# Optimization experiments

Measured on AMD Instinct MI355X. Metric: run time of the kernel, lower is better.

The kernel has to match this reference:

```python
import jax, jax.numpy as jnp
import numpy as np

N = 100000   # nodes
D = 64       # padded neighbor-list width (avg degree)
F = 256      # in_channels
H = 256      # hidden_channels
E = 131072   # number of target edges
OUT = 1      # out_channels


def _linear_params(key, fin, fout):
    k1, k2 = jax.random.split(key)
    s = 1.0 / np.sqrt(fin)
    w = jax.random.uniform(k1, (fin, fout), jnp.float32, -s, s)
    b = jax.random.uniform(k2, (fout,), jnp.float32, -s, s)
    return w, b


def setup_inputs() -> dict:
    key = jax.random.key(0)
    ks = jax.random.split(key, 12)
    x = jax.random.normal(ks[0], (N, F), jnp.float32)
    # sorted padded neighbor lists: row i -> D neighbor ids (sorted, as in the
    # bit-packed sorted-element representation the torch code intersects)
    neighbors = jnp.sort(jax.random.randint(ks[1], (N, D), 0, N), axis=1).astype(jnp.int32)
    tar_ei = jax.random.randint(ks[2], (2, E), 0, N).astype(jnp.int32)
    cn_w1, cn_b1 = _linear_params(ks[3], 1, H)
    cn_w2, cn_b2 = _linear_params(ks[4], H, H)
    cn_w3, cn_b3 = _linear_params(ks[5], H, H)
    ij_w1, ij_b1 = _linear_params(ks[6], F, H)
    ij_w2, ij_b2 = _linear_params(ks[7], H, H)
    lin_w1, lin_b1 = _linear_params(ks[8], H, H)
    lin_w2, lin_b2 = _linear_params(ks[9], H, OUT)
    beta = jnp.ones((1,), jnp.float32)
    return dict(x=x, neighbors=neighbors, tar_ei=tar_ei, beta=beta,
                cn_w1=cn_w1, cn_b1=cn_b1, cn_w2=cn_w2, cn_b2=cn_b2,
                cn_w3=cn_w3, cn_b3=cn_b3,
                ij_w1=ij_w1, ij_b1=ij_b1, ij_w2=ij_w2, ij_b2=ij_b2,
                lin_w1=lin_w1, lin_b1=lin_b1, lin_w2=lin_w2, lin_b2=lin_b2)


def reference(x, neighbors, tar_ei, beta,
              cn_w1, cn_b1, cn_w2, cn_b2, cn_w3, cn_b3,
              ij_w1, ij_b1, ij_w2, ij_b2,
              lin_w1, lin_b1, lin_w2, lin_b2):
    src, dst = tar_ei[0], tar_ei[1]
    xi = x[src]                       # [E, F] irregular gather
    xj = x[dst]                       # [E, F]

    # adjoverlap / spmoverlap_: per edge, |N(i) ∩ N(j)| via sorted-set
    # intersection; cn.sum(dim=-1) with fill value 1.0 -> CN count.
    ni = neighbors[src]               # [E, D]
    nj = neighbors[dst]               # [E, D]
    matches = ni[:, :, None] == nj[:, None, :]          # [E, D, D]
    xcn = jnp.sum(matches, axis=(1, 2)).astype(jnp.float32)[:, None]  # [E, 1]

    # xcnlin: Linear(1,H) -> ReLU -> Linear(H,H) -> ReLU -> Linear(H,H)
    h = jax.nn.relu(xcn @ cn_w1 + cn_b1)
    h = jax.nn.relu(h @ cn_w2 + cn_b2)
    xcn_feat = h @ cn_w3 + cn_b3                         # [E, H]

    # xijlin: Linear(F,H) -> ReLU -> Linear(H,H)
    g = jax.nn.relu((xi * xj) @ ij_w1 + ij_b1)
    xij = g @ ij_w2 + ij_b2                              # [E, H]

    # lin: Linear(H,H) -> ReLU -> Linear(H,OUT)
    z = jax.nn.relu((xcn_feat * beta + xij) @ lin_w1 + lin_b1)
    out = z @ lin_w2 + lin_b2                            # [E, OUT]
    return out
```

## Files before the change

### kernel.cpp

```cpp
#include <hip/hip_runtime.h>
#include <hip/hip_bf16.h>
#include <stdint.h>

#define EE 131072
#define DDEG 64

typedef __bf16 bf16_t;
typedef bf16_t bf16x8 __attribute__((ext_vector_type(8)));
typedef float floatx4 __attribute__((ext_vector_type(4)));

__global__ __launch_bounds__(256)
void pre_kernel(const int* __restrict__ nbr, const int* __restrict__ tar,
                int* __restrict__ xcn,
                const float* __restrict__ ij_w1, bf16_t* __restrict__ Wt1,
                const float* __restrict__ w2, const float* __restrict__ lw1,
                bf16_t* __restrict__ Mt,
                const float* __restrict__ b2, const float* __restrict__ lb1,
                float* __restrict__ cvec,
                const float* __restrict__ cw1, const float* __restrict__ cb1,
                const float* __restrict__ cw2, const float* __restrict__ cb2,
                const float* __restrict__ cw3, const float* __restrict__ cb3,
                const float* __restrict__ beta, float* __restrict__ T2) {
    __shared__ __align__(16) char arena[33792];
    const int bid = blockIdx.x;
    const int t = threadIdx.x;

    if (bid >= 1088) {
        int wid  = (bid - 1088) * 4 + (t >> 6);
        int lane = t & 63;
        int s = __builtin_amdgcn_readfirstlane(tar[wid]);
        int d = __builtin_amdgcn_readfirstlane(tar[EE + wid]);
        int a = nbr[(size_t)s * DDEG + lane];
        const int* __restrict__ brow = nbr + (size_t)d * DDEG;
        int cnt = 0;
        #pragma unroll
        for (int k = 0; k < 64; ++k)
            cnt += __builtin_popcountll(__ballot(a == brow[k]));
        if (lane == 0) xcn[wid] = cnt;
        return;
    }

    if (bid < 64) {
        float (*tile)[33] = (float (*)[33])arena;
        int bx = bid & 7, by = bid >> 3;
        int tx = t & 31, ty = t >> 5;
        #pragma unroll
        for (int r = 0; r < 32; r += 8)
            tile[ty + r][tx] = ij_w1[(by * 32 + ty + r) * 256 + bx * 32 + tx];
        __syncthreads();
        #pragma unroll
        for (int r = 0; r < 32; r += 8)
            Wt1[(bx * 32 + ty + r) * 256 + by * 32 + tx] = (bf16_t)tile[tx][ty + r];
    } else if (bid < 320) {
        float (*S)[33] = (float (*)[33])arena;
        int b = bid - 64;
        int cc = t & 31, abase = t >> 5;
        float acc = 0.f;
        for (int c0 = 0; c0 < 256; c0 += 32) {
            __syncthreads();
            #pragma unroll
            for (int r = 0; r < 32; ++r) {
                int a = r * 8 + abase;
                S[a][cc] = w2[a * 256 + c0 + cc];
            }
            __syncthreads();
            #pragma unroll 8
            for (int c2 = 0; c2 < 32; ++c2) {
                float wv = lw1[(c0 + c2) * 256 + b];
                acc += S[t][c2] * wv;
            }
        }
        Mt[(size_t)b * 256 + t] = (bf16_t)acc;
    } else if (bid < 576) {
        float* red = (float*)arena;
        int b = bid - 320;
        red[t] = b2[t] * lw1[t * 256 + b];
        __syncthreads();
        for (int s = 128; s > 0; s >>= 1) {
            if (t < s) red[t] += red[t + s];
            __syncthreads();
        }
        if (t == 0) cvec[b] = red[0] + lb1[b];
    } else {
        float* t1 = (float*)arena;
        float* t2 = (float*)(arena + 1024);
        float* t3 = (float*)(arena + 2048);
        int v = bid - 576;
        float fv = (float)v;
        t1[t] = fmaxf(fv * cw1[t] + cb1[t], 0.f);
        __syncthreads();
        float s = cb2[t];
        for (int k = 0; k < 256; ++k) s += t1[k] * cw2[k * 256 + t];
        t2[t] = fmaxf(s, 0.f);
        __syncthreads();
        s = cb3[t];
        for (int k = 0; k < 256; ++k) s += t2[k] * cw3[k * 256 + t];
        t3[t] = s * beta[0];
        __syncthreads();
        s = 0.f;
        for (int k = 0; k < 256; ++k) s += t3[k] * lw1[k * 256 + t];
        T2[(size_t)v * 256 + t] = s;
    }
}

__global__ __launch_bounds__(256, 4)
void fused_kernel(const float* __restrict__ x, const int* __restrict__ tar,
                  const bf16_t* __restrict__ Wt1, const float* __restrict__ b1,
                  const bf16_t* __restrict__ Mt, const float* __restrict__ cvec,
                  const float* __restrict__ T2, const int* __restrict__ xcn,
                  const float* __restrict__ w2, const float* __restrict__ b2s,
                  float* __restrict__ out) {
    __shared__ __align__(16) bf16_t X[64 * 264];
    __shared__ float rowacc[64];

    const int tid  = threadIdx.x;
    const int lane = tid & 63;
    const int wc   = tid >> 6;
    const int quad = lane >> 4;
    const int l16  = lane & 15;
    const int e0   = blockIdx.x * 64;

    {
        const int srow   = tid >> 2;
        const int skbase = (tid & 3) * 8;
        int e = e0 + srow;
        const float* xi = x + (size_t)tar[e] * 256;
        const float* xj = x + (size_t)tar[EE + e] * 256;
        #pragma unroll 2
        for (int kc = 0; kc < 8; ++kc) {
            int k0 = kc * 32 + skbase;
            float4 u0 = *(const float4*)(xi + k0);
            float4 u1 = *(const float4*)(xi + k0 + 4);
            float4 v0 = *(const float4*)(xj + k0);
            float4 v1 = *(const float4*)(xj + k0 + 4);
            bf16x8 p;
            p[0] = (bf16_t)(u0.x * v0.x); p[1] = (bf16_t)(u0.y * v0.y);
            p[2] = (bf16_t)(u0.z * v0.z); p[3] = (bf16_t)(u0.w * v0.w);
            p[4] = (bf16_t)(u1.x * v1.x); p[5] = (bf16_t)(u1.y * v1.y);
            p[6] = (bf16_t)(u1.z * v1.z); p[7] = (bf16_t)(u1.w * v1.w);
            *(bf16x8*)&X[srow * 264 + k0] = p;
        }
    }

    floatx4 acc[4][4];
    #pragma unroll
    for (int i = 0; i < 4; ++i)
        #pragma unroll
        for (int j = 0; j < 4; ++j)
            acc[i][j] = (floatx4){0.f, 0.f, 0.f, 0.f};

    __syncthreads();

    #pragma unroll 2
    for (int kc = 0; kc < 8; ++kc) {
        const int k0 = kc * 32 + quad * 8;
        bf16x8 af[4], bfr[4];
        #pragma unroll
        for (int j = 0; j < 4; ++j)
            bfr[j] = *(const bf16x8*)(Wt1 + (size_t)(wc * 64 + j * 16 + l16) * 256 + k0);
        #pragma unroll
        for (int i = 0; i < 4; ++i)
            af[i] = *(const bf16x8*)(&X[(i * 16 + l16) * 264 + k0]);
        #pragma unroll
        for (int i = 0; i < 4; ++i)
            #pragma unroll
            for (int j = 0; j < 4; ++j)
                acc[i][j] = __builtin_amdgcn_mfma_f32_16x16x32_bf16(
                                af[i], bfr[j], acc[i][j], 0, 0, 0);
    }

    __syncthreads();

    #pragma unroll
    for (int j = 0; j < 4; ++j) {
        int col  = wc * 64 + j * 16 + l16;
        float bv = b1[col];
        #pragma unroll
        for (int i = 0; i < 4; ++i)
            #pragma unroll
            for (int r = 0; r < 4; ++r) {
                int row = i * 16 + quad * 4 + r;
                X[row * 264 + col] = (bf16_t)fmaxf(acc[i][j][r] + bv, 0.f);
            }
    }
    #pragma unroll
    for (int i = 0; i < 4; ++i)
        #pragma unroll
        for (int j = 0; j < 4; ++j)
            acc[i][j] = (floatx4){0.f, 0.f, 0.f, 0.f};
    if (tid < 64) rowacc[tid] = 0.f;

    __syncthreads();

    #pragma unroll 2
    for (int kc = 0; kc < 8; ++kc) {
        const int k0 = kc * 32 + quad * 8;
        bf16x8 af[4], bfr[4];
        #pragma unroll
        for (int j = 0; j < 4; ++j)
            bfr[j] = *(const bf16x8*)(Mt + (size_t)(wc * 64 + j * 16 + l16) * 256 + k0);
        #pragma unroll
        for (int i = 0; i < 4; ++i)
            af[i] = *(const bf16x8*)(&X[(i * 16 + l16) * 264 + k0]);
        #pragma unroll
        for (int i = 0; i < 4; ++i)
            #pragma unroll
            for (int j = 0; j < 4; ++j)
                acc[i][j] = __builtin_amdgcn_mfma_f32_16x16x32_bf16(
                                af[i], bfr[j], acc[i][j], 0, 0, 0);
    }

    int xv[16];
    #pragma unroll
    for (int i = 0; i < 4; ++i)
        #pragma unroll
        for (int r = 0; r < 4; ++r)
            xv[i * 4 + r] = xcn[e0 + i * 16 + quad * 4 + r];

    float pr[16];
    #pragma unroll
    for (int t = 0; t < 16; ++t) pr[t] = 0.f;
    #pragma unroll
    for (int j = 0; j < 4; ++j) {
        int col  = wc * 64 + j * 16 + l16;
        float cv = cvec[col];
        float wv = w2[col];
        #pragma unroll
        for (int i = 0; i < 4; ++i)
            #pragma unroll
            for (int r = 0; r < 4; ++r) {
                float t2v = T2[(size_t)xv[i * 4 + r] * 256 + col];
                float v = fmaxf(acc[i][j][r] + cv + t2v, 0.f);
                pr[i * 4 + r] += v * wv;
            }
    }
    #pragma unroll
    for (int off = 1; off < 16; off <<= 1)
        #pragma unroll
        for (int t = 0; t < 16; ++t)
            pr[t] += __shfl_xor(pr[t], off, 64);
    if (l16 == 0) {
        #pragma unroll
        for (int i = 0; i < 4; ++i)
            #pragma unroll
            for (int r = 0; r < 4; ++r)
                atomicAdd(&rowacc[i * 16 + quad * 4 + r], pr[i * 4 + r]);
    }
    __syncthreads();
    if (tid < 64) out[e0 + tid] = rowacc[tid] + b2s[0];
}

extern "C" void kernel_launch(void* const* d_in, const int* in_sizes, int n_in,
                              void* d_out, int out_size, void* d_ws, size_t ws_size,
                              hipStream_t stream) {
    const float* x      = (const float*)d_in[0];
    const int*   nbr    = (const int*)  d_in[1];
    const int*   tar    = (const int*)  d_in[2];
    const float* beta   = (const float*)d_in[3];
    const float* cn_w1  = (const float*)d_in[4];
    const float* cn_b1  = (const float*)d_in[5];
    const float* cn_w2  = (const float*)d_in[6];
    const float* cn_b2  = (const float*)d_in[7];
    const float* cn_w3  = (const float*)d_in[8];
    const float* cn_b3  = (const float*)d_in[9];
    const float* ij_w1  = (const float*)d_in[10];
    const float* ij_b1  = (const float*)d_in[11];
    const float* ij_w2  = (const float*)d_in[12];
    const float* ij_b2  = (const float*)d_in[13];
    const float* lin_w1 = (const float*)d_in[14];
    const float* lin_b1 = (const float*)d_in[15];
    const float* lin_w2 = (const float*)d_in[16];
    const float* lin_b2 = (const float*)d_in[17];

    char* ws = (char*)d_ws;
    float*  T2    = (float*) (ws + 0);
    int*    xcn   = (int*)   (ws + 524288);
    bf16_t* Wt1   = (bf16_t*)(ws + 1048576);
    bf16_t* Mt    = (bf16_t*)(ws + 1179648);
    float*  cvec  = (float*) (ws + 1310720);

    pre_kernel<<<1088 + EE / 4, 256, 0, stream>>>(
        nbr, tar, xcn, ij_w1, Wt1, ij_w2, lin_w1, Mt,
        ij_b2, lin_b1, cvec,
        cn_w1, cn_b1, cn_w2, cn_b2, cn_w3, cn_b3, beta, T2);
    fused_kernel<<<EE / 64, 256, 0, stream>>>(x, tar, Wt1, ij_b1, Mt, cvec,
                                              T2, xcn, lin_w2, lin_b2,
                                              (float*)d_out);
}
```

Before: 390.9 us.

## Pre-convert node features to bf16 and split CN count into its own kernel

Adds a pass that converts the full x matrix (100000x256) to bf16 once, so the fused kernel gathers half as many bytes per edge (two rows per edge across 131072 edges). The common-neighbor intersection moves into a separate kernel, and the fused kernel loads all gathered chunks up front before multiplying. The conversion costs a full read of x (~100MB) plus a bf16 write (~50MB), which may rival the gather savings. xcn indices are also clamped to 511 as a safety bound for the T2 table lookup.

```diff
diff --git a/kernel.cpp b/kernel.cpp
--- a/kernel.cpp
+++ b/kernel.cpp
@@ -10,33 +10,49 @@
 typedef float floatx4 __attribute__((ext_vector_type(4)));
 
 __global__ __launch_bounds__(256)
-void pre_kernel(const int* __restrict__ nbr, const int* __restrict__ tar,
-                int* __restrict__ xcn,
-                const float* __restrict__ ij_w1, bf16_t* __restrict__ Wt1,
-                const float* __restrict__ w2, const float* __restrict__ lw1,
-                bf16_t* __restrict__ Mt,
-                const float* __restrict__ b2, const float* __restrict__ lb1,
-                float* __restrict__ cvec,
-                const float* __restrict__ cw1, const float* __restrict__ cb1,
-                const float* __restrict__ cw2, const float* __restrict__ cb2,
-                const float* __restrict__ cw3, const float* __restrict__ cb3,
-                const float* __restrict__ beta, float* __restrict__ T2) {
+void cn_kernel(const int* __restrict__ nbr, const int* __restrict__ tar,
+               int* __restrict__ xcn) {
+    int wid  = (blockIdx.x * 256 + threadIdx.x) >> 6;
+    int lane = threadIdx.x & 63;
+    int s = __builtin_amdgcn_readfirstlane(tar[wid]);
+    int d = __builtin_amdgcn_readfirstlane(tar[EE + wid]);
+    int a = nbr[(size_t)s * DDEG + lane];
+    const int* __restrict__ brow = nbr + (size_t)d * DDEG;
+    int cnt = 0;
+    #pragma unroll
+    for (int k = 0; k < 64; ++k)
+        cnt += __builtin_popcountll(__ballot(a == brow[k]));
+    if (lane == 0) xcn[wid] = cnt;
+}
+
+__global__ __launch_bounds__(256)
+void prep_kernel(const float* __restrict__ x, bf16_t* __restrict__ xb,
+                 const float* __restrict__ ij_w1, bf16_t* __restrict__ Wt1,
+                 const float* __restrict__ w2, const float* __restrict__ lw1,
+                 bf16_t* __restrict__ Mt,
+                 const float* __restrict__ b2, const float* __restrict__ lb1,
+                 float* __restrict__ cvec,
+                 const float* __restrict__ cw1, const float* __restrict__ cb1,
+                 const float* __restrict__ cw2, const float* __restrict__ cb2,
+                 const float* __restrict__ cw3, const float* __restrict__ cb3,
+                 const float* __restrict__ beta, float* __restrict__ T2) {
     __shared__ __align__(16) char arena[33792];
     const int bid = blockIdx.x;
     const int t = threadIdx.x;
 
     if (bid >= 1088) {
-        int wid  = (bid - 1088) * 4 + (t >> 6);
-        int lane = t & 63;
-        int s = __builtin_amdgcn_readfirstlane(tar[wid]);
-        int d = __builtin_amdgcn_readfirstlane(tar[EE + wid]);
-        int a = nbr[(size_t)s * DDEG + lane];
-        const int* __restrict__ brow = nbr + (size_t)d * DDEG;
-        int cnt = 0;
-        #pragma unroll
-        for (int k = 0; k < 64; ++k)
-            cnt += __builtin_popcountll(__ballot(a == brow[k]));
-        if (lane == 0) xcn[wid] = cnt;
+        size_t base = (size_t)(bid - 1088) * 4096 + (size_t)t * 16;
+        float4 a0 = *(const float4*)(x + base);
+        float4 a1 = *(const float4*)(x + base + 4);
+        float4 a2 = *(const float4*)(x + base + 8);
+        float4 a3 = *(const float4*)(x + base + 12);
+        bf16x8 o0, o1;
+        o0[0] = (bf16_t)a0.x; o0[1] = (bf16_t)a0.y; o0[2] = (bf16_t)a0.z; o0[3] = (bf16_t)a0.w;
+        o0[4] = (bf16_t)a1.x; o0[5] = (bf16_t)a1.y; o0[6] = (bf16_t)a1.z; o0[7] = (bf16_t)a1.w;
+        o1[0] = (bf16_t)a2.x; o1[1] = (bf16_t)a2.y; o1[2] = (bf16_t)a2.z; o1[3] = (bf16_t)a2.w;
+        o1[4] = (bf16_t)a3.x; o1[5] = (bf16_t)a3.y; o1[6] = (bf16_t)a3.z; o1[7] = (bf16_t)a3.w;
+        *(bf16x8*)(xb + base)     = o0;
+        *(bf16x8*)(xb + base + 8) = o1;
         return;
     }
 
@@ -104,7 +120,7 @@
 }
 
 __global__ __launch_bounds__(256, 4)
-void fused_kernel(const float* __restrict__ x, const int* __restrict__ tar,
+void fused_kernel(const bf16_t* __restrict__ xb, const int* __restrict__ tar,
                   const bf16_t* __restrict__ Wt1, const float* __restrict__ b1,
                   const bf16_t* __restrict__ Mt, const float* __restrict__ cvec,
                   const float* __restrict__ T2, const int* __restrict__ xcn,
@@ -124,21 +140,21 @@
         const int srow   = tid >> 2;
         const int skbase = (tid & 3) * 8;
         int e = e0 + srow;
-        const float* xi = x + (size_t)tar[e] * 256;
-        const float* xj = x + (size_t)tar[EE + e] * 256;
-        #pragma unroll 2
+        const bf16_t* xi = xb + (size_t)tar[e] * 256 + skbase;
+        const bf16_t* xj = xb + (size_t)tar[EE + e] * 256 + skbase;
+        bf16x8 ui[8], vj[8];
+        #pragma unroll
         for (int kc = 0; kc < 8; ++kc) {
-            int k0 = kc * 32 + skbase;
-            float4 u0 = *(const float4*)(xi + k0);
-            float4 u1 = *(const float4*)(xi + k0 + 4);
-            float4 v0 = *(const float4*)(xj + k0);
-            float4 v1 = *(const float4*)(xj + k0 + 4);
+            ui[kc] = *(const bf16x8*)(xi + kc * 32);
+            vj[kc] = *(const bf16x8*)(xj + kc * 32);
+        }
+        #pragma unroll
+        for (int kc = 0; kc < 8; ++kc) {
             bf16x8 p;
-            p[0] = (bf16_t)(u0.x * v0.x); p[1] = (bf16_t)(u0.y * v0.y);
-            p[2] = (bf16_t)(u0.z * v0.z); p[3] = (bf16_t)(u0.w * v0.w);
-            p[4] = (bf16_t)(u1.x * v1.x); p[5] = (bf16_t)(u1.y * v1.y);
-            p[6] = (bf16_t)(u1.z * v1.z); p[7] = (bf16_t)(u1.w * v1.w);
-            *(bf16x8*)&X[srow * 264 + k0] = p;
+            #pragma unroll
+            for (int m = 0; m < 8; ++m)
+                p[m] = (bf16_t)((float)ui[kc][m] * (float)vj[kc][m]);
+            *(bf16x8*)&X[srow * 264 + kc * 32 + skbase] = p;
         }
     }
 
@@ -214,8 +230,10 @@
     #pragma unroll
     for (int i = 0; i < 4; ++i)
         #pragma unroll
-        for (int r = 0; r < 4; ++r)
-            xv[i * 4 + r] = xcn[e0 + i * 16 + quad * 4 + r];
+        for (int r = 0; r < 4; ++r) {
+            int v = xcn[e0 + i * 16 + quad * 4 + r];
+            xv[i * 4 + r] = v < 511 ? v : 511;
+        }
 
     float pr[16];
     #pragma unroll
@@ -278,12 +296,14 @@
     bf16_t* Wt1   = (bf16_t*)(ws + 1048576);
     bf16_t* Mt    = (bf16_t*)(ws + 1179648);
     float*  cvec  = (float*) (ws + 1310720);
-
-    pre_kernel<<<1088 + EE / 4, 256, 0, stream>>>(
-        nbr, tar, xcn, ij_w1, Wt1, ij_w2, lin_w1, Mt,
+    bf16_t* xb    = (bf16_t*)(ws + 1312768);
+
+    cn_kernel<<<EE / 4, 256, 0, stream>>>(nbr, tar, xcn);
+    prep_kernel<<<1088 + 6250, 256, 0, stream>>>(
+        x, xb, ij_w1, Wt1, ij_w2, lin_w1, Mt,
         ij_b2, lin_b1, cvec,
         cn_w1, cn_b1, cn_w2, cn_b2, cn_w3, cn_b3, beta, T2);
-    fused_kernel<<<EE / 64, 256, 0, stream>>>(x, tar, Wt1, ij_b1, Mt, cvec,
+    fused_kernel<<<EE / 64, 256, 0, stream>>>(xb, tar, Wt1, ij_b1, Mt, cvec,
                                               T2, xcn, lin_w2, lin_b2,
                                               (float*)d_out);
 }
```

Result: faster. 372.4 us (-4.7%).
